# Optimization experiments

Hardware: AMD Instinct MI355X
Metric: run time of the kernel (lower is better)

Reference implementation:

```python
import jax, jax.numpy as jnp
import numpy as np

B, N, C = 4, 2048, 64   # batch, tokens, num_feat
HS = 512                # hidden_size
H = HS // C             # 8 heads, head_dim = C = 64
EPS = 1e-6


def _ln(x, g, b):
    m = x.mean(-1, keepdims=True)
    v = ((x - m) ** 2).mean(-1, keepdims=True)
    return (x - m) / jnp.sqrt(v + EPS) * g + b


def setup_inputs() -> dict:
    key = jax.random.key(0)
    ks = jax.random.split(key, 8)
    s = 0.02
    return {
        "x": jax.random.normal(ks[0], (B, N, C), jnp.float32),
        "g1": jnp.ones((C,), jnp.float32),
        "be1": jnp.zeros((C,), jnp.float32),
        "Wqkv": jax.random.normal(ks[1], (C, 3 * HS), jnp.float32) * s,
        "bqkv": jnp.zeros((3 * HS,), jnp.float32),
        "Wout": jax.random.normal(ks[2], (HS, C), jnp.float32) * s,
        "bout": jnp.zeros((C,), jnp.float32),
        "g2": jnp.ones((C,), jnp.float32),
        "be2": jnp.zeros((C,), jnp.float32),
        "W1": jax.random.normal(ks[3], (C, HS // 8), jnp.float32) * s,
        "b1": jax.random.normal(ks[4], (HS // 8,), jnp.float32) * 1e-6,
        "W2": jax.random.normal(ks[5], (HS // 8, C), jnp.float32) * s,
        "b2": jax.random.normal(ks[6], (C,), jnp.float32) * 1e-6,
    }


def reference(x, g1, be1, Wqkv, bqkv, Wout, bout, g2, be2, W1, b1, W2, b2):
    b_, n_, c_ = x.shape
    hs = Wout.shape[0]
    h_ = hs // c_
    res = x
    y = _ln(x, g1, be1)
    # fused QKV: (B,N,3*HS) -> (3,B,H,N,D) with D = c_
    qkv = (y @ Wqkv + bqkv).reshape(b_, n_, 3, h_, c_).transpose(2, 0, 3, 1, 4)
    q, k, v = qkv[0], qkv[1], qkv[2]
    scores = jnp.einsum('bhqd,bhkd->bhqk', q, k) / jnp.sqrt(jnp.asarray(c_, x.dtype))
    probs = jax.nn.softmax(scores, axis=-1)
    ctx = jnp.einsum('bhqk,bhkd->bhqd', probs, v)
    ctx = ctx.transpose(0, 2, 1, 3).reshape(b_, n_, hs)
    attn = jax.nn.gelu(ctx @ Wout + bout, approximate=False)  # GELU after out proj per source
    x2 = attn + res
    y2 = _ln(x2, g2, be2)
    mlp = jax.nn.gelu(y2 @ W1 + b1, approximate=False) @ W2 + b2
    return mlp + x2
```

## Files before the change

### kernel.cpp

```cpp
#include <hip/hip_runtime.h>


#define NN 2048
#define CC 64
#define HH 8
#define HSZ 512
#define QKSCALE 0.42466092f

typedef __bf16 bf16x8 __attribute__((ext_vector_type(8)));
typedef float f32x4 __attribute__((ext_vector_type(4)));

__device__ __forceinline__ float b2f(unsigned short u) {
  union { unsigned int i; float f; } v; v.i = ((unsigned int)u) << 16; return v.f;
}
__device__ __forceinline__ unsigned short f2b(float f) {
  union { float f; unsigned int i; } v; v.f = f;
  unsigned int r = v.i + 0x7FFFu + ((v.i >> 16) & 1u);
  return (unsigned short)(r >> 16);
}
__device__ __forceinline__ unsigned int pk2(float a, float b) {
  return (unsigned int)f2b(a) | ((unsigned int)f2b(b) << 16);
}
__device__ __forceinline__ unsigned char f2fp8(float f) {
  int p = __builtin_amdgcn_cvt_pk_fp8_f32(f, f, 0, false);
  return (unsigned char)(p & 0xFF);
}
__device__ __forceinline__ float gelu_f(float x) {
  return 0.5f * x * (1.0f + erff(x * 0.7071067811865475f));
}

__global__ __launch_bounds__(256) void k_ln_qkv(
    const float* __restrict__ x,
    const float* __restrict__ g1,
    const float* __restrict__ be1,
    const float* __restrict__ W,
    const float* __restrict__ bqkv,
    unsigned char* __restrict__ Qb,
    unsigned char* __restrict__ Kb,
    unsigned char* __restrict__ VbT)
{
  __shared__ __align__(16) unsigned short As[64 * 72];
  __shared__ __align__(16) unsigned short Ws[128 * 72];
  const int tid = threadIdx.x, wv = tid >> 6, lane = tid & 63;
  const int col = lane & 15, quad = lane >> 4;
  const int bm = blockIdx.x & 127, bn = blockIdx.x >> 7;
  const int m0 = bm * 64, nw = bn * 128;

  const int c4 = tid & 15;
  float4 gv = *(const float4*)(g1 + c4 * 4);
  float4 bv = *(const float4*)(be1 + c4 * 4);
  #pragma unroll
  for (int s = 0; s < 4; ++s) {
    int idx = s * 256 + tid;
    int row = idx >> 4;
    float4 xv = *(const float4*)(x + (size_t)(m0 + row) * CC + c4 * 4);
    float ps = xv.x + xv.y + xv.z + xv.w;
    float ps2 = xv.x * xv.x + xv.y * xv.y + xv.z * xv.z + xv.w * xv.w;
    #pragma unroll
    for (int off = 8; off; off >>= 1) {
      ps += __shfl_xor(ps, off, 16);
      ps2 += __shfl_xor(ps2, off, 16);
    }
    float mean = ps * (1.0f / 64.0f);
    float var = ps2 * (1.0f / 64.0f) - mean * mean;
    float rs = rsqrtf(var + 1e-6f);
    uint2 packed;
    packed.x = pk2((xv.x - mean) * rs * gv.x + bv.x, (xv.y - mean) * rs * gv.y + bv.y);
    packed.y = pk2((xv.z - mean) * rs * gv.z + bv.z, (xv.w - mean) * rs * gv.w + bv.w);
    *(uint2*)&As[row * 72 + c4 * 4] = packed;
  }

  {
    const int c_loc = tid & 127;
    const int kg = tid >> 7;
    const int ng = nw + c_loc;
    #pragma unroll
    for (int g = 0; g < 4; ++g) {
      float wv8[8];
      #pragma unroll
      for (int j = 0; j < 8; ++j) wv8[j] = W[(size_t)(kg * 32 + g * 8 + j) * 1536 + ng];
      uint4 u;
      u.x = pk2(wv8[0], wv8[1]); u.y = pk2(wv8[2], wv8[3]);
      u.z = pk2(wv8[4], wv8[5]); u.w = pk2(wv8[6], wv8[7]);
      *(uint4*)&Ws[c_loc * 72 + kg * 32 + g * 8] = u;
    }
  }
  __syncthreads();

  bf16x8 af0 = *(const bf16x8*)&As[(wv * 16 + col) * 72 + quad * 8];
  bf16x8 af1 = *(const bf16x8*)&As[(wv * 16 + col) * 72 + 32 + quad * 8];

  f32x4 acc[8];
  #pragma unroll
  for (int nt = 0; nt < 8; ++nt) acc[nt] = (f32x4){0.f, 0.f, 0.f, 0.f};
  #pragma unroll
  for (int nt = 0; nt < 8; ++nt) {
    bf16x8 b0 = *(const bf16x8*)&Ws[(nt * 16 + col) * 72 + quad * 8];
    bf16x8 b1 = *(const bf16x8*)&Ws[(nt * 16 + col) * 72 + 32 + quad * 8];
    acc[nt] = __builtin_amdgcn_mfma_f32_16x16x32_bf16(af0, b0, acc[nt], 0, 0, 0);
    acc[nt] = __builtin_amdgcn_mfma_f32_16x16x32_bf16(af1, b1, acc[nt], 0, 0, 0);
  }

  const int tkb = m0 + wv * 16 + quad * 4;
  const int bb = tkb >> 11;
  const int nnb = tkb & 2047;
  #pragma unroll
  for (int nt = 0; nt < 8; ++nt) {
    const int n0 = nw + nt * 16;
    const int which = n0 >> 9;
    const int h = (n0 >> 6) & 7;
    const int d0 = n0 & 63;
    const float bias = bqkv[n0 + col];
    float vv[4];
    #pragma unroll
    for (int r = 0; r < 4; ++r) vv[r] = acc[nt][r] + bias;
    if (which == 2) {
      int lo = __builtin_amdgcn_cvt_pk_fp8_f32(vv[0], vv[1], 0, false);
      int full = __builtin_amdgcn_cvt_pk_fp8_f32(vv[2], vv[3], lo, true);
      *(unsigned int*)(VbT + ((size_t)(bb * HH + h) * CC + d0 + col) * NN + nnb) =
          (unsigned int)full;
    } else {
      unsigned char* dst = (which == 0) ? Qb : Kb;
      #pragma unroll
      for (int r = 0; r < 4; ++r)
        dst[((size_t)(bb * HH + h) * NN + nnb + r) * CC + d0 + col] =
            f2fp8(vv[r] * QKSCALE);
    }
  }
}

__global__ __launch_bounds__(256) void k_attn(
    const unsigned char* __restrict__ Q,
    const unsigned char* __restrict__ K,
    const unsigned char* __restrict__ VT,
    const float* __restrict__ Wout,
    unsigned short* __restrict__ part,
    float* __restrict__ lsums)
{
  __shared__ __align__(16) unsigned char smem[27648];
  unsigned char* Ks = smem;
  unsigned char* Vt = smem + 5120;
  unsigned short* Wb = (unsigned short*)smem;
  unsigned short* Ob = (unsigned short*)(smem + 9216);
  const int tid = threadIdx.x, wv = tid >> 6, lane = tid & 63;
  const int col = lane & 15, quad = lane >> 4;
  const int bid = blockIdx.x;
  const int tc = bid & 1, qc = (bid >> 1) & 15, bh = bid >> 5;
  const size_t base = (size_t)bh * NN * CC;
  const int q0 = qc * 128 + wv * 32;
  const int t0 = tc * 1024;

  if (tid < 80) {
    unsigned int fill = (tid < 5) ? 0x38383838u : 0u;
    uint4 u; u.x = fill; u.y = fill; u.z = fill; u.w = fill;
    *(uint4*)&Vt[64 * 80 + tid * 16] = u;
  }

  long qf[2][2];
  #pragma unroll
  for (int mt = 0; mt < 2; ++mt)
    #pragma unroll
    for (int kh = 0; kh < 2; ++kh)
      qf[mt][kh] = *(const long*)(Q + base + (size_t)(q0 + mt * 16 + col) * CC + kh * 32 + quad * 8);

  f32x4 o[2][4];
  f32x4 ol[2];
  #pragma unroll
  for (int mt = 0; mt < 2; ++mt) {
    #pragma unroll
    for (int dt = 0; dt < 4; ++dt) o[mt][dt] = (f32x4){0.f, 0.f, 0.f, 0.f};
    ol[mt] = (f32x4){0.f, 0.f, 0.f, 0.f};
  }
  const int sl0 = ((quad & 1) << 5) + col;
  const int sl1 = sl0 + 16;
  const bool hiq = (quad >= 2);

  for (int kt = 0; kt < 16; ++kt) {
    const int tb = t0 + kt * 64;
    {
      int row = tid >> 2, c16 = (tid & 3) << 4;
      *(uint4*)&Ks[row * 80 + c16] = *(const uint4*)(K + base + (size_t)(tb + row) * CC + c16);
      *(uint4*)&Vt[row * 80 + c16] = *(const uint4*)(VT + base + (size_t)row * NN + tb + c16);
    }
    __syncthreads();

    unsigned int Dw[2][4];
    #pragma unroll
    for (int ct = 0; ct < 4; ++ct) {
      long k0 = *(const long*)&Ks[(ct * 16 + col) * 80 + quad * 8];
      long k1 = *(const long*)&Ks[(ct * 16 + col) * 80 + 32 + quad * 8];
      #pragma unroll
      for (int mt = 0; mt < 2; ++mt) {
        f32x4 a = (f32x4){0.f, 0.f, 0.f, 0.f};
        a = __builtin_amdgcn_mfma_f32_16x16x32_fp8_fp8(k0, qf[mt][0], a, 0, 0, 0);
        a = __builtin_amdgcn_mfma_f32_16x16x32_fp8_fp8(k1, qf[mt][1], a, 0, 0, 0);
        float p0 = __builtin_amdgcn_exp2f(a[0]);
        float p1 = __builtin_amdgcn_exp2f(a[1]);
        float p2 = __builtin_amdgcn_exp2f(a[2]);
        float p3 = __builtin_amdgcn_exp2f(a[3]);
        int lo = __builtin_amdgcn_cvt_pk_fp8_f32(p0, p1, 0, false);
        Dw[mt][ct] = (unsigned int)__builtin_amdgcn_cvt_pk_fp8_f32(p2, p3, lo, true);
      }
    }

    #pragma unroll
    for (int kh = 0; kh < 2; ++kh) {
      long pb[2];
      #pragma unroll
      for (int mt = 0; mt < 2; ++mt) {
        unsigned int a0 = (unsigned int)__shfl((int)Dw[mt][2 * kh], sl0, 64);
        unsigned int b0 = (unsigned int)__shfl((int)Dw[mt][2 * kh + 1], sl0, 64);
        unsigned int a1 = (unsigned int)__shfl((int)Dw[mt][2 * kh], sl1, 64);
        unsigned int b1 = (unsigned int)__shfl((int)Dw[mt][2 * kh + 1], sl1, 64);
        unsigned long lo = hiq ? b0 : a0;
        unsigned long hi = hiq ? b1 : a1;
        pb[mt] = (long)(lo | (hi << 32));
      }
      #pragma unroll
      for (int dt = 0; dt < 4; ++dt) {
        long vf = *(const long*)&Vt[(dt * 16 + col) * 80 + kh * 32 + quad * 8];
        o[0][dt] = __builtin_amdgcn_mfma_f32_16x16x32_fp8_fp8(vf, pb[0], o[0][dt], 0, 0, 0);
        o[1][dt] = __builtin_amdgcn_mfma_f32_16x16x32_fp8_fp8(vf, pb[1], o[1][dt], 0, 0, 0);
      }
      long vl = *(const long*)&Vt[(64 + col) * 80 + kh * 32 + quad * 8];
      ol[0] = __builtin_amdgcn_mfma_f32_16x16x32_fp8_fp8(vl, pb[0], ol[0], 0, 0, 0);
      ol[1] = __builtin_amdgcn_mfma_f32_16x16x32_fp8_fp8(vl, pb[1], ol[1], 0, 0, 0);
    }
    __syncthreads();
  }

  const int h = bh & 7, b = bh >> 3;
  #pragma unroll
  for (int mt = 0; mt < 2; ++mt) {
    if (quad == 0)
      lsums[(size_t)(tc * 32 + bh) * NN + q0 + mt * 16 + col] = ol[mt][0];
  }

  {
    const int c = tid & 63, kg = tid >> 6;
    #pragma unroll
    for (int j = 0; j < 16; ++j)
      Wb[c * 72 + kg * 16 + j] = f2b(Wout[(size_t)(h * 64 + kg * 16 + j) * 64 + c]);
  }
  unsigned short* Obw = Ob + wv * (32 * 72);
  #pragma unroll
  for (int mt = 0; mt < 2; ++mt)
    #pragma unroll
    for (int dt = 0; dt < 4; ++dt) {
      uint2 u;
      u.x = pk2(o[mt][dt][0], o[mt][dt][1]);
      u.y = pk2(o[mt][dt][2], o[mt][dt][3]);
      *(uint2*)&Obw[(mt * 16 + col) * 72 + dt * 16 + quad * 4] = u;
    }
  __syncthreads();

  #pragma unroll
  for (int mt = 0; mt < 2; ++mt) {
    bf16x8 oa0 = *(const bf16x8*)&Obw[(mt * 16 + col) * 72 + quad * 8];
    bf16x8 oa1 = *(const bf16x8*)&Obw[(mt * 16 + col) * 72 + 32 + quad * 8];
    #pragma unroll
    for (int nt = 0; nt < 4; ++nt) {
      bf16x8 bw0 = *(const bf16x8*)&Wb[(nt * 16 + col) * 72 + quad * 8];
      bf16x8 bw1 = *(const bf16x8*)&Wb[(nt * 16 + col) * 72 + 32 + quad * 8];
      f32x4 ac = (f32x4){0.f, 0.f, 0.f, 0.f};
      ac = __builtin_amdgcn_mfma_f32_16x16x32_bf16(oa0, bw0, ac, 0, 0, 0);
      ac = __builtin_amdgcn_mfma_f32_16x16x32_bf16(oa1, bw1, ac, 0, 0, 0);
      #pragma unroll
      for (int r = 0; r < 4; ++r) {
        int n = q0 + mt * 16 + quad * 4 + r;
        part[((size_t)(tc * 32 + bh) * NN + n) * CC + nt * 16 + col] = f2b(ac[r]);
      }
    }
  }
}

__global__ __launch_bounds__(256) void k_post(
    const unsigned short* __restrict__ part,
    const float* __restrict__ lsums,
    const float* __restrict__ x,
    const float* __restrict__ bout,
    const float* __restrict__ g2,
    const float* __restrict__ be2,
    const float* __restrict__ W1,
    const float* __restrict__ b1,
    const float* __restrict__ W2,
    const float* __restrict__ b2v,
    float* __restrict__ out)
{
  __shared__ __align__(16) float Ws1[64 * 64];
  __shared__ __align__(16) float Ws2[64 * 64];
  __shared__ float ys[8][64], hs[8][64];
  const int tid = threadIdx.x, wid = tid >> 6, lane = tid & 63;
  const int w2 = wid * 2;
  const int tk0 = blockIdx.x * 8 + w2;

  #pragma unroll
  for (int p = 0; p < 4; ++p) {
    int idx = p * 256 + tid;
    *(float4*)&Ws1[idx * 4] = *(const float4*)(W1 + idx * 4);
    *(float4*)&Ws2[idx * 4] = *(const float4*)(W2 + idx * 4);
  }

  const float boutl = bout[lane];
  const float g2l = g2[lane], be2l = be2[lane];
  float x2v[2];
  #pragma unroll
  for (int t = 0; t < 2; ++t) {
    const int tk = tk0 + t;
    const int b = tk >> 11, n = tk & 2047;
    float proj = 0.f;
    #pragma unroll
    for (int h = 0; h < 8; ++h) {
      size_t i0 = (size_t)(b * HH + h) * NN + n;
      size_t i1 = i0 + (size_t)32 * NN;
      float p = b2f(part[i0 * CC + lane]) + b2f(part[i1 * CC + lane]);
      float l = lsums[i0] + lsums[i1];
      proj += p * __builtin_amdgcn_rcpf(l);
    }
    float a = gelu_f(proj + boutl);
    float x2 = a + x[(size_t)tk * CC + lane];
    x2v[t] = x2;
    float s = x2;
    #pragma unroll
    for (int off = 32; off; off >>= 1) s += __shfl_xor(s, off, 64);
    float mean = s * (1.0f / 64.0f);
    float d = x2 - mean;
    float vs = d * d;
    #pragma unroll
    for (int off = 32; off; off >>= 1) vs += __shfl_xor(vs, off, 64);
    float var = vs * (1.0f / 64.0f);
    ys[w2 + t][lane] = d * rsqrtf(var + 1e-6f) * g2l + be2l;
  }
  __syncthreads();

  float acc2[2] = {0.f, 0.f};
  #pragma unroll 8
  for (int c = 0; c < 64; ++c) {
    float w = Ws1[c * 64 + lane];
    acc2[0] += ys[w2][c] * w;
    acc2[1] += ys[w2 + 1][c] * w;
  }
  const float b1l = b1[lane];
  hs[w2][lane] = gelu_f(acc2[0] + b1l);
  hs[w2 + 1][lane] = gelu_f(acc2[1] + b1l);

  float acc3[2] = {0.f, 0.f};
  #pragma unroll 8
  for (int c = 0; c < 64; ++c) {
    float w = Ws2[c * 64 + lane];
    acc3[0] += hs[w2][c] * w;
    acc3[1] += hs[w2 + 1][c] * w;
  }
  const float b2l = b2v[lane];
  #pragma unroll
  for (int t = 0; t < 2; ++t)
    out[(size_t)(tk0 + t) * CC + lane] = acc3[t] + b2l + x2v[t];
}

extern "C" void kernel_launch(void* const* d_in, const int* in_sizes, int n_in,
                              void* d_out, int out_size, void* d_ws, size_t ws_size,
                              hipStream_t stream) {
  const float* x    = (const float*)d_in[0];
  const float* g1   = (const float*)d_in[1];
  const float* be1  = (const float*)d_in[2];
  const float* Wqkv = (const float*)d_in[3];
  const float* bqkv = (const float*)d_in[4];
  const float* Wout = (const float*)d_in[5];
  const float* bout = (const float*)d_in[6];
  const float* g2   = (const float*)d_in[7];
  const float* be2  = (const float*)d_in[8];
  const float* W1   = (const float*)d_in[9];
  const float* b1   = (const float*)d_in[10];
  const float* W2   = (const float*)d_in[11];
  const float* b2   = (const float*)d_in[12];
  float* out = (float*)d_out;

  unsigned char* wsb = (unsigned char*)d_ws;
  const size_t SZ = (size_t)4 * HH * NN * CC;
  unsigned char* Qb   = wsb;
  unsigned char* Kb   = wsb + SZ;
  unsigned char* VbT  = wsb + 2 * SZ;
  unsigned short* part = (unsigned short*)(wsb + 3 * SZ);
  float* lsums         = (float*)(wsb + 3 * SZ + 4 * SZ);

  k_ln_qkv<<<1536, 256, 0, stream>>>(x, g1, be1, Wqkv, bqkv, Qb, Kb, VbT);
  k_attn<<<1024, 256, 0, stream>>>(Qb, Kb, VbT, Wout, part, lsums);
  k_post<<<1024, 256, 0, stream>>>(part, lsums, x, bout, g2, be2, W1, b1, W2, b2, out);
}
```

Measured before the change: 152.3 us.

## Stage QKV stores through LDS, double-buffer attention K/V tiles, bf16 MLP weights

The QKV kernel's epilogue now writes fp8 Q/K/V tiles into shared memory first and then issues coalesced 16-byte global stores, replacing scattered byte and strided stores. The attention kernel double-buffers K/V tiles: it prefetches the next tile into registers during compute and drops one barrier per iteration, at the cost of twice the tile LDS. The post kernel keeps W1/W2 in LDS as bf16 instead of fp32, halving that LDS footprint but rounding the MLP weights to bf16.

```diff
diff --git a/kernel.cpp b/kernel.cpp
--- a/kernel.cpp
+++ b/kernel.cpp
@@ -41,6 +41,7 @@
 {
   __shared__ __align__(16) unsigned short As[64 * 72];
   __shared__ __align__(16) unsigned short Ws[128 * 72];
+  unsigned char* Es = (unsigned char*)As;
   const int tid = threadIdx.x, wv = tid >> 6, lane = tid & 63;
   const int col = lane & 15, quad = lane >> 4;
   const int bm = blockIdx.x & 127, bn = blockIdx.x >> 7;
@@ -100,31 +101,46 @@
     acc[nt] = __builtin_amdgcn_mfma_f32_16x16x32_bf16(af0, b0, acc[nt], 0, 0, 0);
     acc[nt] = __builtin_amdgcn_mfma_f32_16x16x32_bf16(af1, b1, acc[nt], 0, 0, 0);
   }
-
-  const int tkb = m0 + wv * 16 + quad * 4;
-  const int bb = tkb >> 11;
-  const int nnb = tkb & 2047;
-  #pragma unroll
-  for (int nt = 0; nt < 8; ++nt) {
-    const int n0 = nw + nt * 16;
-    const int which = n0 >> 9;
-    const int h = (n0 >> 6) & 7;
-    const int d0 = n0 & 63;
-    const float bias = bqkv[n0 + col];
-    float vv[4];
-    #pragma unroll
-    for (int r = 0; r < 4; ++r) vv[r] = acc[nt][r] + bias;
-    if (which == 2) {
-      int lo = __builtin_amdgcn_cvt_pk_fp8_f32(vv[0], vv[1], 0, false);
-      int full = __builtin_amdgcn_cvt_pk_fp8_f32(vv[2], vv[3], lo, true);
-      *(unsigned int*)(VbT + ((size_t)(bb * HH + h) * CC + d0 + col) * NN + nnb) =
-          (unsigned int)full;
-    } else {
-      unsigned char* dst = (which == 0) ? Qb : Kb;
+  __syncthreads();
+
+  const int bb = m0 >> 11;
+  const int nloc = m0 & 2047;
+  const int which = nw >> 9;
+  const int hbase = (nw >> 6) & 7;
+  const int tloc = wv * 16 + quad * 4;
+
+  if (which == 2) {
+    #pragma unroll
+    for (int nt = 0; nt < 8; ++nt) {
+      const int hb = nt >> 2, d0 = (nt & 3) * 16;
+      const float bias = bqkv[nw + nt * 16 + col];
+      int lo = __builtin_amdgcn_cvt_pk_fp8_f32(acc[nt][0] + bias, acc[nt][1] + bias, 0, false);
+      int full = __builtin_amdgcn_cvt_pk_fp8_f32(acc[nt][2] + bias, acc[nt][3] + bias, lo, true);
+      *(unsigned int*)&Es[hb * 4096 + (d0 + col) * 64 + tloc] = (unsigned int)full;
+    }
+    __syncthreads();
+    const int d = tid >> 2, nseg = (tid & 3) * 16;
+    #pragma unroll
+    for (int hb = 0; hb < 2; ++hb) {
+      size_t off = ((size_t)(bb * HH + hbase + hb) * CC + d) * NN + nloc + nseg;
+      *(uint4*)(VbT + off) = *(const uint4*)&Es[hb * 4096 + tid * 16];
+    }
+  } else {
+    const float scale = (which == 0) ? QKSCALE : 1.0f;
+    #pragma unroll
+    for (int nt = 0; nt < 8; ++nt) {
+      const int hb = nt >> 2, d0 = (nt & 3) * 16;
+      const float bias = bqkv[nw + nt * 16 + col];
       #pragma unroll
       for (int r = 0; r < 4; ++r)
-        dst[((size_t)(bb * HH + h) * NN + nnb + r) * CC + d0 + col] =
-            f2fp8(vv[r] * QKSCALE);
+        Es[hb * 4096 + (tloc + r) * 64 + d0 + col] = f2fp8((acc[nt][r] + bias) * scale);
+    }
+    __syncthreads();
+    unsigned char* dst = (which == 0) ? Qb : Kb;
+    #pragma unroll
+    for (int hb = 0; hb < 2; ++hb) {
+      size_t off = ((size_t)(bb * HH + hbase + hb) * NN + nloc) * CC + tid * 16;
+      *(uint4*)(dst + off) = *(const uint4*)&Es[hb * 4096 + tid * 16];
     }
   }
 }
@@ -138,8 +154,6 @@
     float* __restrict__ lsums)
 {
   __shared__ __align__(16) unsigned char smem[27648];
-  unsigned char* Ks = smem;
-  unsigned char* Vt = smem + 5120;
   unsigned short* Wb = (unsigned short*)smem;
   unsigned short* Ob = (unsigned short*)(smem + 9216);
   const int tid = threadIdx.x, wv = tid >> 6, lane = tid & 63;
@@ -149,11 +163,13 @@
   const size_t base = (size_t)bh * NN * CC;
   const int q0 = qc * 128 + wv * 32;
   const int t0 = tc * 1024;
-
-  if (tid < 80) {
-    unsigned int fill = (tid < 5) ? 0x38383838u : 0u;
+  const int srow = tid >> 2, sc16 = (tid & 3) << 4;
+
+  if (tid < 160) {
+    int bsel = tid >= 80, t2 = tid - bsel * 80;
+    unsigned int fill = (t2 < 5) ? 0x38383838u : 0u;
     uint4 u; u.x = fill; u.y = fill; u.z = fill; u.w = fill;
-    *(uint4*)&Vt[64 * 80 + tid * 16] = u;
+    *(uint4*)&smem[bsel * 11520 + 5120 + 64 * 80 + t2 * 16] = u;
   }
 
   long qf[2][2];
@@ -175,14 +191,24 @@
   const int sl1 = sl0 + 16;
   const bool hiq = (quad >= 2);
 
+  {
+    *(uint4*)&smem[srow * 80 + sc16] =
+        *(const uint4*)(K + base + (size_t)(t0 + srow) * CC + sc16);
+    *(uint4*)&smem[5120 + srow * 80 + sc16] =
+        *(const uint4*)(VT + base + (size_t)srow * NN + t0 + sc16);
+  }
+  __syncthreads();
+
   for (int kt = 0; kt < 16; ++kt) {
-    const int tb = t0 + kt * 64;
-    {
-      int row = tid >> 2, c16 = (tid & 3) << 4;
-      *(uint4*)&Ks[row * 80 + c16] = *(const uint4*)(K + base + (size_t)(tb + row) * CC + c16);
-      *(uint4*)&Vt[row * 80 + c16] = *(const uint4*)(VT + base + (size_t)row * NN + tb + c16);
-    }
-    __syncthreads();
+    unsigned char* Ks = smem + (kt & 1) * 11520;
+    unsigned char* Vt = Ks + 5120;
+    uint4 kreg, vreg;
+    const bool more = (kt + 1) < 16;
+    if (more) {
+      const int tb2 = t0 + (kt + 1) * 64;
+      kreg = *(const uint4*)(K + base + (size_t)(tb2 + srow) * CC + sc16);
+      vreg = *(const uint4*)(VT + base + (size_t)srow * NN + tb2 + sc16);
+    }
 
     unsigned int Dw[2][4];
     #pragma unroll
@@ -225,6 +251,12 @@
       long vl = *(const long*)&Vt[(64 + col) * 80 + kh * 32 + quad * 8];
       ol[0] = __builtin_amdgcn_mfma_f32_16x16x32_fp8_fp8(vl, pb[0], ol[0], 0, 0, 0);
       ol[1] = __builtin_amdgcn_mfma_f32_16x16x32_fp8_fp8(vl, pb[1], ol[1], 0, 0, 0);
+    }
+
+    if (more) {
+      unsigned char* Kn = smem + ((kt + 1) & 1) * 11520;
+      *(uint4*)&Kn[srow * 80 + sc16] = kreg;
+      *(uint4*)&Kn[5120 + srow * 80 + sc16] = vreg;
     }
     __syncthreads();
   }
@@ -287,8 +319,8 @@
     const float* __restrict__ b2v,
     float* __restrict__ out)
 {
-  __shared__ __align__(16) float Ws1[64 * 64];
-  __shared__ __align__(16) float Ws2[64 * 64];
+  __shared__ __align__(16) unsigned short Ws1[64 * 64];
+  __shared__ __align__(16) unsigned short Ws2[64 * 64];
   __shared__ float ys[8][64], hs[8][64];
   const int tid = threadIdx.x, wid = tid >> 6, lane = tid & 63;
   const int w2 = wid * 2;
@@ -297,8 +329,12 @@
   #pragma unroll
   for (int p = 0; p < 4; ++p) {
     int idx = p * 256 + tid;
-    *(float4*)&Ws1[idx * 4] = *(const float4*)(W1 + idx * 4);
-    *(float4*)&Ws2[idx * 4] = *(const float4*)(W2 + idx * 4);
+    float4 a1 = *(const float4*)(W1 + idx * 4);
+    float4 a2 = *(const float4*)(W2 + idx * 4);
+    uint2 u1; u1.x = pk2(a1.x, a1.y); u1.y = pk2(a1.z, a1.w);
+    uint2 u2; u2.x = pk2(a2.x, a2.y); u2.y = pk2(a2.z, a2.w);
+    *(uint2*)&Ws1[idx * 4] = u1;
+    *(uint2*)&Ws2[idx * 4] = u2;
   }
 
   const float boutl = bout[lane];
@@ -336,7 +372,7 @@
   float acc2[2] = {0.f, 0.f};
   #pragma unroll 8
   for (int c = 0; c < 64; ++c) {
-    float w = Ws1[c * 64 + lane];
+    float w = b2f(Ws1[c * 64 + lane]);
     acc2[0] += ys[w2][c] * w;
     acc2[1] += ys[w2 + 1][c] * w;
   }
@@ -347,7 +383,7 @@
   float acc3[2] = {0.f, 0.f};
   #pragma unroll 8
   for (int c = 0; c < 64; ++c) {
-    float w = Ws2[c * 64 + lane];
+    float w = b2f(Ws2[c * 64 + lane]);
     acc3[0] += hs[w2][c] * w;
     acc3[1] += hs[w2 + 1][c] * w;
   }
```

Result: no change. 152.6 us (+0.2%).
